# Optimization experiments

Measured on AMD Instinct MI355X. Metric: run time of the kernel, lower is better.

The kernel has to match this reference:

```python
import jax, jax.numpy as jnp
import numpy as np
import math

B, L, S, D = 4, 4096, 4096, 256
EPS = 1e-5

def _layernorm(x, g, b):
    mu = jnp.mean(x, axis=-1, keepdims=True)
    var = jnp.mean(jnp.square(x - mu), axis=-1, keepdims=True)
    return (x - mu) * jax.lax.rsqrt(var + EPS) * g + b

def setup_inputs() -> dict:
    key = jax.random.key(0)
    ks = jax.random.split(key, 14)
    s = 1.0 / math.sqrt(D)
    s2 = 1.0 / math.sqrt(2 * D)
    inp = {
        "source": jax.random.normal(ks[0], (B, L, D), jnp.float32),
        "target": jax.random.normal(ks[1], (B, S, D), jnp.float32),
        # linear weights stored as [in, out]
        "Wq": jax.random.uniform(ks[2], (D, D), jnp.float32, -s, s),
        "bq": jnp.zeros((D,), jnp.float32),
        "Wk": jax.random.uniform(ks[3], (D, D), jnp.float32, -s, s),
        "bk": jnp.zeros((D,), jnp.float32),
        "Wv": jax.random.uniform(ks[4], (D, D), jnp.float32, -s, s),
        "bv": jnp.zeros((D,), jnp.float32),
        "Wm": jax.random.uniform(ks[5], (D, D), jnp.float32, -s, s),
        "bm": jnp.zeros((D,), jnp.float32),
        "g1": jnp.ones((D,), jnp.float32),
        "beta1": jnp.zeros((D,), jnp.float32),
        "W1": jax.random.uniform(ks[6], (2 * D, 2 * D), jnp.float32, -s2, s2),
        "W2": jax.random.uniform(ks[7], (2 * D, D), jnp.float32, -s2, s2),
        "g2": jnp.ones((D,), jnp.float32),
        "beta2": jnp.zeros((D,), jnp.float32),
    }
    return inp

def reference(source, target, Wq, bq, Wk, bk, Wv, bv, Wm, bm, g1, beta1, W1, W2, g2, beta2):
    q = source @ Wq + bq              # [B, L, D]
    k = target @ Wk + bk              # [B, S, D]
    v = target @ Wv + bv              # [B, S, D]
    scale = 1.0 / math.sqrt(D)
    scores = jnp.einsum("bld,bsd->bls", q, k) * scale   # [B, L, S] materialized, as in source
    attn = jax.nn.softmax(scores, axis=-1)
    message = jnp.einsum("bls,bsd->bld", attn, v)        # [B, L, D]
    message = message @ Wm + bm
    message = _layernorm(message, g1, beta1)
    h = jnp.concatenate([source, message], axis=-1)      # [B, L, 2D]
    h = jax.nn.gelu(h @ W1, approximate=False)           # torch GELU is exact erf
    message = _layernorm(h @ W2, g2, beta2)
    return source + message
```

## Files before the change

### kernel.cpp

```cpp
#include <hip/hip_runtime.h>

typedef __bf16 bf16x8 __attribute__((ext_vector_type(8)));
typedef float f32x16 __attribute__((ext_vector_type(16)));
typedef float f32x4 __attribute__((ext_vector_type(4)));
typedef unsigned int u32;
typedef unsigned int u32x4 __attribute__((ext_vector_type(4)));
typedef unsigned short u16;
typedef unsigned short u16x4 __attribute__((ext_vector_type(4)));
typedef unsigned short u16x8 __attribute__((ext_vector_type(8)));

#define DEV static __device__ __forceinline__
#define AS1 __attribute__((address_space(1)))
#define AS3 __attribute__((address_space(3)))

DEV u16 f2bf(float f){
  unsigned u = __float_as_uint(f);
  u += 0x7FFFu + ((u >> 16) & 1u);
  return (u16)(u >> 16);
}
DEV float bf2f(u16 h){ return __uint_as_float(((u32)h) << 16); }

DEV void stage16(const u16* gsrc, const u16* ldst){
  __builtin_amdgcn_global_load_lds((const AS1 u32*)(unsigned long long)gsrc,
                                   (AS3 u32*)(u32)(unsigned long long)ldst,
                                   16, 0, 0);
}

constexpr int BATCH = 4, LQ = 4096, SK = 4096, DH = 256, BL = BATCH * LQ;
constexpr int NHALF = 2;
constexpr int ITERS = SK / NHALF / 64;

__global__ void prep_weights(const float* __restrict__ Wq, const float* __restrict__ Wk,
                             const float* __restrict__ Wv, const float* __restrict__ Wm,
                             const float* __restrict__ W1, const float* __restrict__ W2,
                             const float* __restrict__ bk, const float* __restrict__ bv,
                             u16* __restrict__ WqT, u16* __restrict__ WkvT,
                             u16* __restrict__ WmT,
                             u16* __restrict__ W1T, u16* __restrict__ W2T,
                             float* __restrict__ bkv){
  int idx = blockIdx.x * 256 + threadIdx.x;
  if (idx < 262144){
    int which = idx >> 16, i2 = idx & 65535;
    int r = i2 >> 8, c = i2 & 255;
    const float* S = (which==0)?Wq:(which==1)?Wk:(which==2)?Wv:Wm;
    u16*         D = (which==0)?WqT:(which==1)?WkvT:(which==2)?(WkvT+65536):WmT;
    D[c*256 + r] = f2bf(S[i2]);
  } else if (idx < 524288){
    int i2 = idx - 262144;
    int r = i2 >> 9, c = i2 & 511;
    W1T[c*512 + r] = f2bf(W1[i2]);
  } else if (idx < 655360){
    int i2 = idx - 524288;
    int r = i2 >> 8, c = i2 & 255;
    W2T[(size_t)c*512 + r] = f2bf(W2[i2]);
  } else if (idx < 655872){
    int i2 = idx - 655360;
    bkv[i2] = (i2 < 256) ? bk[i2] : bv[i2 - 256];
  }
}

template<bool A_F32, int EPI, bool WH>
__global__ __launch_bounds__(256, 2) void gemm128(
  const void* __restrict__ Ap, int lda, const u16* __restrict__ BTp,
  const float* __restrict__ bias, void* __restrict__ outp, void* __restrict__ outp2,
  u16* __restrict__ hcat,
  int M, int N, int K, float scale)
{
  __shared__ u16 A_lds[128 * 64];
  __shared__ u16 B_lds[128 * 64];
  const int tid = threadIdx.x, lane = tid & 63, wid = tid >> 6;
  const int ql = lane & 31, g = lane >> 5;
  const int m0 = blockIdx.y * 128, n0 = blockIdx.x * 128;
  const int mr = (wid & 1) * 64, nr = (wid >> 1) * 64;

  f32x16 acc[2][2] = {};
  f32x4 afreg[8];
  u32x4 abreg[4];
  u32x4 breg[4];
  const float* Af = (const float*)Ap;
  const u16*   Ab = (const u16*)Ap;

#define G_LOAD_A(kb) do { \
    if constexpr (A_F32){ \
      _Pragma("unroll") \
      for (int i = 0; i < 8; i++){ int item = tid + i*256; int r = item>>4, c = (item&15)*4; \
        afreg[i] = *(const f32x4*)&Af[(size_t)(m0+r)*lda + (kb)*64 + c]; } \
    } else { \
      _Pragma("unroll") \
      for (int i = 0; i < 4; i++){ int item = tid + i*256; int r = item>>3, c = (item&7)*8; \
        abreg[i] = *(const u32x4*)&Ab[(size_t)(m0+r)*lda + (kb)*64 + c]; } \
    } \
  } while(0)
#define G_LOAD_B(kb) do { \
    _Pragma("unroll") \
    for (int i = 0; i < 4; i++){ int item = tid + i*256; int r = item>>3, c = (item&7)*8; \
      breg[i] = *(const u32x4*)&BTp[(size_t)(n0+r)*K + (kb)*64 + c]; } \
  } while(0)

  G_LOAD_A(0); G_LOAD_B(0);

  const int nkb = K >> 6;
  for (int kb = 0; kb < nkb; ++kb){
    __syncthreads();
    if constexpr (A_F32){
      #pragma unroll
      for (int i = 0; i < 8; i++){ int item = tid + i*256; int r = item>>4, c = (item&15)*4;
        u16x4 h; h[0]=f2bf(afreg[i][0]); h[1]=f2bf(afreg[i][1]);
                 h[2]=f2bf(afreg[i][2]); h[3]=f2bf(afreg[i][3]);
        *(u16x4*)&A_lds[r*64 + (c ^ ((r&7)*8))] = h;
        if constexpr (WH){
          if (n0 == 0) *(u16x4*)&hcat[(size_t)(m0+r)*512 + kb*64 + c] = h;
        }
      }
    } else {
      #pragma unroll
      for (int i = 0; i < 4; i++){ int item = tid + i*256; int r = item>>3, c = (item&7)*8;
        *(u32x4*)&A_lds[r*64 + (c ^ ((r&7)*8))] = abreg[i]; }
    }
    #pragma unroll
    for (int i = 0; i < 4; i++){ int item = tid + i*256; int r = item>>3, c = (item&7)*8;
      *(u32x4*)&B_lds[r*64 + (c ^ ((r&7)*8))] = breg[i]; }
    __syncthreads();
    if (kb + 1 < nkb){ G_LOAD_A(kb+1); G_LOAD_B(kb+1); }

    #pragma unroll
    for (int kk = 0; kk < 4; kk++){
      bf16x8 af[2], bf[2];
      #pragma unroll
      for (int mi = 0; mi < 2; mi++)
        af[mi] = __builtin_bit_cast(bf16x8,
          *(const u32x4*)&A_lds[(mr+mi*32+ql)*64 + ((kk*16+g*8) ^ ((ql&7)*8))]);
      #pragma unroll
      for (int ni = 0; ni < 2; ni++)
        bf[ni] = __builtin_bit_cast(bf16x8,
          *(const u32x4*)&B_lds[(nr+ni*32+ql)*64 + ((kk*16+g*8) ^ ((ql&7)*8))]);
      #pragma unroll
      for (int mi = 0; mi < 2; mi++)
        #pragma unroll
        for (int ni = 0; ni < 2; ni++)
          acc[mi][ni] = __builtin_amdgcn_mfma_f32_32x32x16_bf16(af[mi], bf[ni], acc[mi][ni], 0, 0, 0);
    }
  }

  #pragma unroll
  for (int mi = 0; mi < 2; mi++){
    #pragma unroll
    for (int ni = 0; ni < 2; ni++){
      const int col = n0 + nr + ni*32 + ql;
      const float bv = bias ? bias[col] : 0.f;
      if constexpr (EPI == 4){
        if (col < 256){
          #pragma unroll
          for (int j = 0; j < 16; j++){
            int row = m0 + mr + mi*32 + (j&3) + 8*(j>>2) + 4*g;
            ((u16*)outp)[(size_t)row*256 + col] = f2bf(acc[mi][ni][j] + bv);
          }
        } else {
          const int col2 = col - 256;
          #pragma unroll
          for (int qd = 0; qd < 4; qd++){
            u16x4 h;
            #pragma unroll
            for (int i = 0; i < 4; i++) h[i] = f2bf(acc[mi][ni][qd*4+i] + bv);
            int row0 = m0 + mr + mi*32 + qd*8 + 4*g;
            int bb = row0 >> 12, ss = row0 & 4095;
            *(u16x4*)&((u16*)outp2)[((size_t)bb*DH + col2)*SK + ss] = h;
          }
        }
      } else {
        #pragma unroll
        for (int j = 0; j < 16; j++){
          int row = m0 + mr + mi*32 + (j&3) + 8*(j>>2) + 4*g;
          ((u16*)outp)[(size_t)row*N + col] = f2bf((acc[mi][ni][j] + bv) * scale);
        }
      }
    }
  }
}

__global__ __launch_bounds__(256, 2) void gemm_ln_wm(
  const u16* __restrict__ opart, const float* __restrict__ stats,
  const u16* __restrict__ BTp, const float* __restrict__ bias,
  const float* __restrict__ gamma, const float* __restrict__ beta,
  u16* __restrict__ outp)
{
  constexpr int K = 256;
  __shared__ __align__(16) char smem[36864];
  u16* A_lds = (u16*)smem;
  u16* B_lds = (u16*)(smem + 4096);
  float* scratch = (float*)smem;

  const int tid = threadIdx.x, lane = tid & 63, wid = tid >> 6;
  const int ql = lane & 31, g = lane >> 5;
  const int m0 = blockIdx.x * 32;
  const int ar = tid >> 3, ac = (tid & 7) * 8;

  float winv;
  { int row = m0 + ar;
    winv = 1.f / (stats[row] + stats[(size_t)BL + row]); }

  f32x16 acc[2] = {};
  u32x4 areg, areg2;
  u32x4 breg[8];

#define WM_LOAD_A(kb) do { \
    areg  = *(const u32x4*)&opart[(size_t)(m0+ar)*DH + (kb)*64 + ac]; \
    areg2 = *(const u32x4*)&opart[(size_t)BL*DH + (size_t)(m0+ar)*DH + (kb)*64 + ac]; \
  } while(0)
#define WM_LOAD_B(kb) do { \
    _Pragma("unroll") \
    for (int i = 0; i < 8; i++){ int item = tid + i*256; int r = item>>3, c = (item&7)*8; \
      breg[i] = *(const u32x4*)&BTp[(size_t)r*K + (kb)*64 + c]; } \
  } while(0)

  WM_LOAD_A(0); WM_LOAD_B(0);

  const int nkb = K >> 6;
  for (int kb = 0; kb < nkb; ++kb){
    __syncthreads();
    { u16x8 h;
      #pragma unroll
      for (int e = 0; e < 8; e++){
        u16 h0 = (u16)(areg[e>>1]  >> ((e&1)*16));
        u16 h1 = (u16)(areg2[e>>1] >> ((e&1)*16));
        h[e] = f2bf((bf2f(h0) + bf2f(h1)) * winv);
      }
      *(u16x8*)&A_lds[ar*64 + (ac ^ ((ar&7)*8))] = h; }
    #pragma unroll
    for (int i = 0; i < 8; i++){ int item = tid + i*256; int r = item>>3, c = (item&7)*8;
      *(u32x4*)&B_lds[r*64 + (c ^ ((r&7)*8))] = breg[i]; }
    __syncthreads();
    if (kb + 1 < nkb){ WM_LOAD_A(kb+1); WM_LOAD_B(kb+1); }

    #pragma unroll
    for (int kk = 0; kk < 4; kk++){
      bf16x8 af = __builtin_bit_cast(bf16x8,
        *(const u32x4*)&A_lds[ql*64 + ((kk*16+g*8) ^ ((ql&7)*8))]);
      #pragma unroll
      for (int ni = 0; ni < 2; ni++){
        bf16x8 bf = __builtin_bit_cast(bf16x8,
          *(const u32x4*)&B_lds[(wid*64+ni*32+ql)*64 + ((kk*16+g*8) ^ ((ql&7)*8))]);
        acc[ni] = __builtin_amdgcn_mfma_f32_32x32x16_bf16(af, bf, acc[ni], 0, 0, 0);
      }
    }
  }

  __syncthreads();

  float bv0 = bias[wid*64 + ql], bv1 = bias[wid*64 + 32 + ql];
  #pragma unroll
  for (int ni = 0; ni < 2; ni++)
    #pragma unroll
    for (int j = 0; j < 16; j++){
      int row = (j&3) + 8*(j>>2) + 4*g;
      scratch[row*257 + wid*64 + ni*32 + ql] = acc[ni][j] + (ni ? bv1 : bv0);
    }
  __syncthreads();

  f32x4 gv = *(const f32x4*)&gamma[lane*4];
  f32x4 bvv = *(const f32x4*)&beta[lane*4];
  #pragma unroll
  for (int rr = 0; rr < 8; rr++){
    const int row = wid*8 + rr;
    f32x4 v = *(const f32x4*)&scratch[row*257 + lane*4];
    float s1 = v[0]+v[1]+v[2]+v[3];
    float s2 = v[0]*v[0]+v[1]*v[1]+v[2]*v[2]+v[3]*v[3];
    #pragma unroll
    for (int m = 1; m < 64; m <<= 1){ s1 += __shfl_xor(s1, m, 64); s2 += __shfl_xor(s2, m, 64); }
    float mu = s1 * (1.f/DH);
    float var = s2 * (1.f/DH) - mu*mu;
    float rstd = rsqrtf(var + 1e-5f);
    u16x4 h;
    #pragma unroll
    for (int i = 0; i < 4; i++) h[i] = f2bf((v[i]-mu)*rstd*gv[i] + bvv[i]);
    *(u16x4*)&outp[(size_t)(m0+row)*512 + 256 + lane*4] = h;
  }
}

__global__ __launch_bounds__(256, 2) void fused_mlp(
  const u16* __restrict__ hcat, const u16* __restrict__ W1T,
  const u16* __restrict__ W2T, const float* __restrict__ gamma,
  const float* __restrict__ beta, const float* __restrict__ src,
  float* __restrict__ outp)
{
  __shared__ __align__(16) char smem[69632];
  u16* A1 = (u16*)smem;
  u16* B1 = (u16*)(smem + 4096);
  u16* Hl = (u16*)smem;
  u16* B2 = (u16*)(smem + 36864);
  float* scratch = (float*)smem;

  const int tid = threadIdx.x, lane = tid & 63, wid = tid >> 6;
  const int ql = lane & 31, g = lane >> 5;
  const int m0 = blockIdx.x * 32;

  f32x16 acc1[4] = {};
  for (int kb = 0; kb < 8; ++kb){
    if (kb) __syncthreads();
    { int r = tid >> 3, slot = tid & 7;
      stage16(&hcat[(size_t)(m0+r)*512 + kb*64 + ((slot ^ (r&7))<<3)],
              &A1[tid*8]); }
    #pragma unroll
    for (int i = 0; i < 16; i++){
      int grp = tid + i*256; int r = grp>>3, slot = grp&7;
      stage16(&W1T[(size_t)r*512 + kb*64 + ((slot ^ (r&7))<<3)], &B1[grp*8]);
    }
    __syncthreads();
    #pragma unroll
    for (int kk = 0; kk < 4; kk++){
      bf16x8 af = __builtin_bit_cast(bf16x8,
        *(const u32x4*)&A1[ql*64 + ((kk*16+g*8) ^ ((ql&7)*8))]);
      #pragma unroll
      for (int ni = 0; ni < 4; ni++){
        int rB = wid*128 + ni*32 + ql;
        bf16x8 bf = __builtin_bit_cast(bf16x8,
          *(const u32x4*)&B1[rB*64 + ((kk*16+g*8) ^ ((rB&7)*8))]);
        acc1[ni] = __builtin_amdgcn_mfma_f32_32x32x16_bf16(af, bf, acc1[ni], 0, 0, 0);
      }
    }
  }
  __syncthreads();

  #pragma unroll
  for (int ni = 0; ni < 4; ni++){
    const int col = wid*128 + ni*32 + ql;
    const int s = col >> 3;
    #pragma unroll
    for (int j = 0; j < 16; j++){
      int row = (j&3) + 8*(j>>2) + 4*g;
      float v = acc1[ni][j];
      v = 0.5f * v * (1.f + erff(v * 0.70710678118f));
      Hl[row*512 + ((s ^ (row&7))<<3) + (col&7)] = f2bf(v);
    }
  }
  __syncthreads();

  f32x16 acc2[2] = {};
  for (int kb = 0; kb < 8; ++kb){
    if (kb) __syncthreads();
    #pragma unroll
    for (int i = 0; i < 8; i++){
      int grp = tid + i*256; int r = grp>>3, slot = grp&7;
      stage16(&W2T[(size_t)r*512 + kb*64 + ((slot ^ (r&7))<<3)], &B2[grp*8]);
    }
    __syncthreads();
    #pragma unroll
    for (int kk = 0; kk < 4; kk++){
      int c0 = kb*64 + kk*16 + g*8;
      bf16x8 af = __builtin_bit_cast(bf16x8,
        *(const u32x4*)&Hl[ql*512 + (((c0>>3) ^ (ql&7))<<3)]);
      #pragma unroll
      for (int ni = 0; ni < 2; ni++){
        int rB = wid*64 + ni*32 + ql;
        bf16x8 bf = __builtin_bit_cast(bf16x8,
          *(const u32x4*)&B2[rB*64 + ((kk*16+g*8) ^ ((rB&7)*8))]);
        acc2[ni] = __builtin_amdgcn_mfma_f32_32x32x16_bf16(af, bf, acc2[ni], 0, 0, 0);
      }
    }
  }
  __syncthreads();

  #pragma unroll
  for (int ni = 0; ni < 2; ni++)
    #pragma unroll
    for (int j = 0; j < 16; j++){
      int row = (j&3) + 8*(j>>2) + 4*g;
      scratch[row*257 + wid*64 + ni*32 + ql] = acc2[ni][j];
    }
  __syncthreads();

  f32x4 gv = *(const f32x4*)&gamma[lane*4];
  f32x4 bvv = *(const f32x4*)&beta[lane*4];
  #pragma unroll
  for (int rr = 0; rr < 8; rr++){
    const int row = wid*8 + rr;
    f32x4 v = *(const f32x4*)&scratch[row*257 + lane*4];
    float s1 = v[0]+v[1]+v[2]+v[3];
    float s2 = v[0]*v[0]+v[1]*v[1]+v[2]*v[2]+v[3]*v[3];
    #pragma unroll
    for (int m = 1; m < 64; m <<= 1){ s1 += __shfl_xor(s1, m, 64); s2 += __shfl_xor(s2, m, 64); }
    float mu = s1 * (1.f/DH);
    float var = s2 * (1.f/DH) - mu*mu;
    float rstd = rsqrtf(var + 1e-5f);
    f32x4 s = *(const f32x4*)&src[(size_t)(m0+row)*DH + lane*4];
    f32x4 o;
    #pragma unroll
    for (int i = 0; i < 4; i++) o[i] = s[i] + (v[i]-mu)*rstd*gv[i] + bvv[i];
    *(f32x4*)&outp[(size_t)(m0+row)*DH + lane*4] = o;
  }
}

__global__ __launch_bounds__(512, 2) void attn_kernel(
  const u16* __restrict__ qb, const u16* __restrict__ kb,
  const u16* __restrict__ vtb, u16* __restrict__ opart, float* __restrict__ stats)
{
  __shared__ u16 K_lds[2][64 * 256];
  __shared__ u16 VT_lds[2][256 * 64];
  __shared__ u32x4 P_exch[4][4][64];
  __shared__ float L_exch[4][2][32];

  const int tid = threadIdx.x;
  const int wid = tid >> 6, lane = tid & 63;
  const int ql = lane & 31, g = lane >> 5;
  const int qpair = wid >> 1, sh = wid & 1;
  const int b = blockIdx.y, half = blockIdx.z;
  const int qrow0 = blockIdx.x * 128 + qpair * 32;
  const int s0base = half * (SK / NHALF);

  const u16* kbase = kb  + (size_t)b * SK * DH;
  const u16* vbase = vtb + (size_t)b * DH * SK;

#define STAGE_K(bi, s0) do { \
    _Pragma("unroll") \
    for (int i = 0; i < 4; i++){ \
      int grp = tid + i*512; int s = grp>>5, slot = grp&31; \
      stage16(kbase + (size_t)((s0)+s)*DH + ((slot ^ (s&31))<<3), \
              &K_lds[bi][(i*512 + wid*64)*8]); \
    } } while(0)
#define STAGE_V(bi, s0) do { \
    _Pragma("unroll") \
    for (int i = 0; i < 4; i++){ \
      int grp = tid + i*512; int d = grp>>3, slot = grp&7; \
      stage16(vbase + (size_t)d*SK + (s0) + ((slot ^ (d&7))<<3), \
              &VT_lds[bi][(i*512 + wid*64)*8]); \
    } } while(0)

  STAGE_K(0, s0base);
  STAGE_V(0, s0base);

  bf16x8 qf[16];
  {
    const u16* qp = qb + ((size_t)(b*LQ + qrow0 + ql)) * DH + g * 8;
    #pragma unroll
    for (int kk = 0; kk < 16; kk++)
      qf[kk] = __builtin_bit_cast(bf16x8, *(const u32x4*)(qp + kk*16));
  }

  f32x16 accO[4] = {};
  float l_lane = 0.f;

  __syncthreads();

  for (int it = 0; it < ITERS; ++it){
    const int cur = it & 1;
    if (it + 1 < ITERS){
      STAGE_K(cur ^ 1, s0base + (it+1)*64);
      STAGE_V(cur ^ 1, s0base + (it+1)*64);
    }

    f32x16 ps = {};
    __builtin_amdgcn_s_setprio(1);
    #pragma unroll
    for (int kk = 0; kk < 16; ++kk){
      bf16x8 kf = __builtin_bit_cast(bf16x8,
        *(const u32x4*)&K_lds[cur][(sh*32+ql)*256 + (((kk*2+g) ^ ql)<<3)]);
      ps = __builtin_amdgcn_mfma_f32_32x32x16_bf16(kf, qf[kk], ps, 0, 0, 0);
    }
    __builtin_amdgcn_s_setprio(0);

    #pragma unroll
    for (int j = 0; j < 16; j++) ps[j] = exp2f(ps[j]);
    float s8[8];
    #pragma unroll
    for (int j = 0; j < 8; j++) s8[j] = ps[j] + ps[j+8];
    l_lane += ((s8[0]+s8[4]) + (s8[1]+s8[5])) + ((s8[2]+s8[6]) + (s8[3]+s8[7]));

    u32 Wp[4][2];
    #pragma unroll
    for (int qd = 0; qd < 4; qd++)
      #pragma unroll
      for (int h = 0; h < 2; h++){
        float lo = ps[qd*4 + 2*h], hi = ps[qd*4 + 2*h + 1];
        asm("v_cvt_pk_bf16_f32 %0, %1, %2" : "=v"(Wp[qd][h]) : "v"(lo), "v"(hi));
      }
    #pragma unroll
    for (int i = 0; i < 2; i++){
      const int qp2 = i * 2;
      u32 a0 = Wp[qp2][0], b0 = Wp[qp2+1][0];
      u32 a1 = Wp[qp2][1], b1 = Wp[qp2+1][1];
      asm("v_permlane32_swap_b32 %0, %1" : "+v"(a0), "+v"(b0));
      asm("v_permlane32_swap_b32 %0, %1" : "+v"(a1), "+v"(b1));
      u32x4 w; w[0] = a0; w[1] = a1; w[2] = b0; w[3] = b1;
      P_exch[qpair][sh*2 + i][lane] = w;
    }

    asm volatile("s_waitcnt lgkmcnt(0)" ::: "memory");
    __builtin_amdgcn_s_barrier();
    __builtin_amdgcn_sched_barrier(0);

    bf16x8 pf0 = __builtin_bit_cast(bf16x8, P_exch[qpair][0][lane]);
    bf16x8 pf1 = __builtin_bit_cast(bf16x8, P_exch[qpair][1][lane]);
    bf16x8 pf2 = __builtin_bit_cast(bf16x8, P_exch[qpair][2][lane]);
    bf16x8 pf3 = __builtin_bit_cast(bf16x8, P_exch[qpair][3][lane]);

    __builtin_amdgcn_s_setprio(1);
    #pragma unroll
    for (int dt = 0; dt < 4; dt++){
      const int dtg = sh*4 + dt;
      bf16x8 vf0 = __builtin_bit_cast(bf16x8,
        *(const u32x4*)&VT_lds[cur][(dtg*32+ql)*64 + (((0*2+g) ^ (ql&7))<<3)]);
      accO[dt] = __builtin_amdgcn_mfma_f32_32x32x16_bf16(vf0, pf0, accO[dt], 0, 0, 0);
      bf16x8 vf1 = __builtin_bit_cast(bf16x8,
        *(const u32x4*)&VT_lds[cur][(dtg*32+ql)*64 + (((1*2+g) ^ (ql&7))<<3)]);
      accO[dt] = __builtin_amdgcn_mfma_f32_32x32x16_bf16(vf1, pf1, accO[dt], 0, 0, 0);
      bf16x8 vf2 = __builtin_bit_cast(bf16x8,
        *(const u32x4*)&VT_lds[cur][(dtg*32+ql)*64 + (((2*2+g) ^ (ql&7))<<3)]);
      accO[dt] = __builtin_amdgcn_mfma_f32_32x32x16_bf16(vf2, pf2, accO[dt], 0, 0, 0);
      bf16x8 vf3 = __builtin_bit_cast(bf16x8,
        *(const u32x4*)&VT_lds[cur][(dtg*32+ql)*64 + (((3*2+g) ^ (ql&7))<<3)]);
      accO[dt] = __builtin_amdgcn_mfma_f32_32x32x16_bf16(vf3, pf3, accO[dt], 0, 0, 0);
    }
    __builtin_amdgcn_s_setprio(0);

    asm volatile("s_waitcnt vmcnt(0) lgkmcnt(0)" ::: "memory");
    __builtin_amdgcn_s_barrier();
    __builtin_amdgcn_sched_barrier(0);
  }

  float l_run = l_lane + __shfl_xor(l_lane, 32, 64);
  if (g == 0) L_exch[qpair][sh][ql] = l_run;
  __syncthreads();
  float l_tot = l_run + L_exch[qpair][sh^1][ql];

  const int rowb = b * LQ + qrow0;
  if (sh == 0 && g == 0)
    stats[(size_t)half*BL + rowb + ql] = l_tot;

  float* scratch = (float*)&K_lds[0][0] + wid * 1056;
  #pragma unroll
  for (int dt = 0; dt < 4; dt++){
    const int dtg = sh*4 + dt;
    #pragma unroll
    for (int j = 0; j < 16; j++){
      int dl = (j&3) + 8*(j>>2) + 4*g;
      scratch[ql*33 + dl] = accO[dt][j];
    }
    int q2 = lane >> 1, dl2 = (lane & 1) * 16;
    u16x8 h0, h1;
    #pragma unroll
    for (int i = 0; i < 8; i++){ h0[i] = f2bf(scratch[q2*33 + dl2 + i]);
                                 h1[i] = f2bf(scratch[q2*33 + dl2 + 8 + i]); }
    u16* op = &opart[((size_t)half*BL + rowb + q2)*DH + dtg*32 + dl2];
    *(u16x8*)op = h0;
    *(u16x8*)(op + 8) = h1;
  }
}

extern "C" void kernel_launch(void* const* d_in, const int* in_sizes, int n_in,
                              void* d_out, int out_size, void* d_ws, size_t ws_size,
                              hipStream_t stream)
{
  const float* source = (const float*)d_in[0];
  const float* target = (const float*)d_in[1];
  const float* Wq = (const float*)d_in[2];  const float* bq = (const float*)d_in[3];
  const float* Wk = (const float*)d_in[4];  const float* bk = (const float*)d_in[5];
  const float* Wv = (const float*)d_in[6];  const float* bv = (const float*)d_in[7];
  const float* Wm = (const float*)d_in[8];  const float* bm = (const float*)d_in[9];
  const float* g1 = (const float*)d_in[10]; const float* be1 = (const float*)d_in[11];
  const float* W1 = (const float*)d_in[12]; const float* W2 = (const float*)d_in[13];
  const float* g2 = (const float*)d_in[14]; const float* be2 = (const float*)d_in[15];

  char* ws = (char*)d_ws;
  u16* WqT  = (u16*)(ws);
  u16* WkvT = (u16*)(ws + (size_t)(1u<<17));
  u16* WmT  = (u16*)(ws + (size_t)3*(1u<<17));
  u16* W1T  = (u16*)(ws + (size_t)4*(1u<<17));
  u16* W2T  = (u16*)(ws + (size_t)8*(1u<<17));
  float* bkv = (float*)(ws + (size_t)10*(1u<<17));
  size_t off = (size_t)10*(1u<<17) + 4096;
  u16* qbuf  = (u16*)(ws + off); off += (size_t)BL*DH*2;
  u16* kbuf  = (u16*)(ws + off); off += (size_t)BL*DH*2;
  u16* vtbuf = (u16*)(ws + off); off += (size_t)BL*DH*2;
  u16* hcat  = (u16*)(ws + off); off += (size_t)BL*512*2;
  u16* opart = (u16*)(ws + off); off += (size_t)NHALF*BL*DH*2;
  float* stats = (float*)(ws + off); off += (size_t)NHALF*BL*4;

  prep_weights<<<dim3(2562), 256, 0, stream>>>(Wq, Wk, Wv, Wm, W1, W2, bk, bv,
                                               WqT, WkvT, WmT, W1T, W2T, bkv);

  const float qscale = 1.4426950408889634f / 16.0f;
  gemm128<true, 0, true><<<dim3(2, BL/128), 256, 0, stream>>>(
      source, 256, WqT, bq, qbuf, nullptr, hcat, BL, 256, 256, qscale);
  gemm128<true, 4, false><<<dim3(4, BL/128), 256, 0, stream>>>(
      target, 256, WkvT, bkv, kbuf, vtbuf, nullptr, BL, 512, 256, 1.0f);

  attn_kernel<<<dim3(LQ/128, BATCH, NHALF), 512, 0, stream>>>(qbuf, kbuf, vtbuf, opart, stats);

  gemm_ln_wm<<<dim3(BL/32), 256, 0, stream>>>(opart, stats, WmT, bm, g1, be1, hcat);

  fused_mlp<<<dim3(BL/32), 256, 0, stream>>>(hcat, W1T, W2T, g2, be2, source,
                                             (float*)d_out);
}
```

Before: 162.8 us.

## Merge Q and KV projection launches; double row tile in Wm and MLP kernels

The separate Q and KV projection GEMM launches become one qkv_gemm launch. Blocks pick source/Wq or target/Wkv from blockIdx.x, which cuts one launch and fills the GPU better. The Wm+LayerNorm and fused MLP kernels move from 32-row, 256-thread blocks to 64-row, 512-thread blocks, so each weight tile staged into LDS is reused across twice as many rows. The cost is larger LDS use (up to 96KB) and bigger blocks, which may lower occupancy and halves the grid size.

```diff
diff --git a/kernel.cpp b/kernel.cpp
--- a/kernel.cpp
+++ b/kernel.cpp
@@ -59,69 +59,57 @@
   }
 }
 
-template<bool A_F32, int EPI, bool WH>
-__global__ __launch_bounds__(256, 2) void gemm128(
-  const void* __restrict__ Ap, int lda, const u16* __restrict__ BTp,
-  const float* __restrict__ bias, void* __restrict__ outp, void* __restrict__ outp2,
-  u16* __restrict__ hcat,
-  int M, int N, int K, float scale)
+__global__ __launch_bounds__(256, 2) void qkv_gemm(
+  const float* __restrict__ src, const float* __restrict__ tgt,
+  const u16* __restrict__ WqT, const u16* __restrict__ WkvT,
+  const float* __restrict__ bq, const float* __restrict__ bkv,
+  u16* __restrict__ qbuf, u16* __restrict__ kbuf, u16* __restrict__ vtbuf,
+  u16* __restrict__ hcat, float qscale)
 {
   __shared__ u16 A_lds[128 * 64];
   __shared__ u16 B_lds[128 * 64];
   const int tid = threadIdx.x, lane = tid & 63, wid = tid >> 6;
   const int ql = lane & 31, g = lane >> 5;
-  const int m0 = blockIdx.y * 128, n0 = blockIdx.x * 128;
+  const bool isQ = blockIdx.x < 2;
+  const int m0 = blockIdx.y * 128;
+  const int n0 = (isQ ? blockIdx.x : (blockIdx.x - 2)) * 128;
   const int mr = (wid & 1) * 64, nr = (wid >> 1) * 64;
+  const float* Af = isQ ? src : tgt;
+  const u16* BTp = isQ ? WqT : WkvT;
+  const float* bias = isQ ? bq : bkv;
+  const bool wh = isQ && (blockIdx.x == 0);
 
   f32x16 acc[2][2] = {};
   f32x4 afreg[8];
-  u32x4 abreg[4];
   u32x4 breg[4];
-  const float* Af = (const float*)Ap;
-  const u16*   Ab = (const u16*)Ap;
-
-#define G_LOAD_A(kb) do { \
-    if constexpr (A_F32){ \
-      _Pragma("unroll") \
-      for (int i = 0; i < 8; i++){ int item = tid + i*256; int r = item>>4, c = (item&15)*4; \
-        afreg[i] = *(const f32x4*)&Af[(size_t)(m0+r)*lda + (kb)*64 + c]; } \
-    } else { \
-      _Pragma("unroll") \
-      for (int i = 0; i < 4; i++){ int item = tid + i*256; int r = item>>3, c = (item&7)*8; \
-        abreg[i] = *(const u32x4*)&Ab[(size_t)(m0+r)*lda + (kb)*64 + c]; } \
-    } \
+
+#define QK_LOAD_A(kb) do { \
+    _Pragma("unroll") \
+    for (int i = 0; i < 8; i++){ int item = tid + i*256; int r = item>>4, c = (item&15)*4; \
+      afreg[i] = *(const f32x4*)&Af[(size_t)(m0+r)*256 + (kb)*64 + c]; } \
   } while(0)
-#define G_LOAD_B(kb) do { \
+#define QK_LOAD_B(kb) do { \
     _Pragma("unroll") \
     for (int i = 0; i < 4; i++){ int item = tid + i*256; int r = item>>3, c = (item&7)*8; \
-      breg[i] = *(const u32x4*)&BTp[(size_t)(n0+r)*K + (kb)*64 + c]; } \
+      breg[i] = *(const u32x4*)&BTp[(size_t)(n0+r)*256 + (kb)*64 + c]; } \
   } while(0)
 
-  G_LOAD_A(0); G_LOAD_B(0);
-
-  const int nkb = K >> 6;
-  for (int kb = 0; kb < nkb; ++kb){
+  QK_LOAD_A(0); QK_LOAD_B(0);
+
+  for (int kb = 0; kb < 4; ++kb){
     __syncthreads();
-    if constexpr (A_F32){
-      #pragma unroll
-      for (int i = 0; i < 8; i++){ int item = tid + i*256; int r = item>>4, c = (item&15)*4;
-        u16x4 h; h[0]=f2bf(afreg[i][0]); h[1]=f2bf(afreg[i][1]);
-                 h[2]=f2bf(afreg[i][2]); h[3]=f2bf(afreg[i][3]);
-        *(u16x4*)&A_lds[r*64 + (c ^ ((r&7)*8))] = h;
-        if constexpr (WH){
-          if (n0 == 0) *(u16x4*)&hcat[(size_t)(m0+r)*512 + kb*64 + c] = h;
-        }
-      }
-    } else {
-      #pragma unroll
-      for (int i = 0; i < 4; i++){ int item = tid + i*256; int r = item>>3, c = (item&7)*8;
-        *(u32x4*)&A_lds[r*64 + (c ^ ((r&7)*8))] = abreg[i]; }
+    #pragma unroll
+    for (int i = 0; i < 8; i++){ int item = tid + i*256; int r = item>>4, c = (item&15)*4;
+      u16x4 h; h[0]=f2bf(afreg[i][0]); h[1]=f2bf(afreg[i][1]);
+               h[2]=f2bf(afreg[i][2]); h[3]=f2bf(afreg[i][3]);
+      *(u16x4*)&A_lds[r*64 + (c ^ ((r&7)*8))] = h;
+      if (wh) *(u16x4*)&hcat[(size_t)(m0+r)*512 + kb*64 + c] = h;
     }
     #pragma unroll
     for (int i = 0; i < 4; i++){ int item = tid + i*256; int r = item>>3, c = (item&7)*8;
       *(u32x4*)&B_lds[r*64 + (c ^ ((r&7)*8))] = breg[i]; }
     __syncthreads();
-    if (kb + 1 < nkb){ G_LOAD_A(kb+1); G_LOAD_B(kb+1); }
+    if (kb + 1 < 4){ QK_LOAD_A(kb+1); QK_LOAD_B(kb+1); }
 
     #pragma unroll
     for (int kk = 0; kk < 4; kk++){
@@ -147,52 +135,49 @@
     #pragma unroll
     for (int ni = 0; ni < 2; ni++){
       const int col = n0 + nr + ni*32 + ql;
-      const float bv = bias ? bias[col] : 0.f;
-      if constexpr (EPI == 4){
-        if (col < 256){
-          #pragma unroll
-          for (int j = 0; j < 16; j++){
-            int row = m0 + mr + mi*32 + (j&3) + 8*(j>>2) + 4*g;
-            ((u16*)outp)[(size_t)row*256 + col] = f2bf(acc[mi][ni][j] + bv);
-          }
-        } else {
-          const int col2 = col - 256;
-          #pragma unroll
-          for (int qd = 0; qd < 4; qd++){
-            u16x4 h;
-            #pragma unroll
-            for (int i = 0; i < 4; i++) h[i] = f2bf(acc[mi][ni][qd*4+i] + bv);
-            int row0 = m0 + mr + mi*32 + qd*8 + 4*g;
-            int bb = row0 >> 12, ss = row0 & 4095;
-            *(u16x4*)&((u16*)outp2)[((size_t)bb*DH + col2)*SK + ss] = h;
-          }
-        }
-      } else {
+      const float bv = bias[col];
+      if (isQ){
         #pragma unroll
         for (int j = 0; j < 16; j++){
           int row = m0 + mr + mi*32 + (j&3) + 8*(j>>2) + 4*g;
-          ((u16*)outp)[(size_t)row*N + col] = f2bf((acc[mi][ni][j] + bv) * scale);
+          qbuf[(size_t)row*256 + col] = f2bf((acc[mi][ni][j] + bv) * qscale);
+        }
+      } else if (col < 256){
+        #pragma unroll
+        for (int j = 0; j < 16; j++){
+          int row = m0 + mr + mi*32 + (j&3) + 8*(j>>2) + 4*g;
+          kbuf[(size_t)row*256 + col] = f2bf(acc[mi][ni][j] + bv);
+        }
+      } else {
+        const int col2 = col - 256;
+        #pragma unroll
+        for (int qd = 0; qd < 4; qd++){
+          u16x4 h;
+          #pragma unroll
+          for (int i = 0; i < 4; i++) h[i] = f2bf(acc[mi][ni][qd*4+i] + bv);
+          int row0 = m0 + mr + mi*32 + qd*8 + 4*g;
+          int bb = row0 >> 12, ss = row0 & 4095;
+          *(u16x4*)&vtbuf[((size_t)bb*DH + col2)*SK + ss] = h;
         }
       }
     }
   }
 }
 
-__global__ __launch_bounds__(256, 2) void gemm_ln_wm(
+__global__ __launch_bounds__(512, 2) void gemm_ln_wm(
   const u16* __restrict__ opart, const float* __restrict__ stats,
   const u16* __restrict__ BTp, const float* __restrict__ bias,
   const float* __restrict__ gamma, const float* __restrict__ beta,
   u16* __restrict__ outp)
 {
-  constexpr int K = 256;
-  __shared__ __align__(16) char smem[36864];
+  __shared__ __align__(16) char smem[65792];
   u16* A_lds = (u16*)smem;
-  u16* B_lds = (u16*)(smem + 4096);
+  u16* B_lds = (u16*)(smem + 8192);
   float* scratch = (float*)smem;
 
   const int tid = threadIdx.x, lane = tid & 63, wid = tid >> 6;
   const int ql = lane & 31, g = lane >> 5;
-  const int m0 = blockIdx.x * 32;
+  const int m0 = blockIdx.x * 64;
   const int ar = tid >> 3, ac = (tid & 7) * 8;
 
   float winv;
@@ -201,7 +186,7 @@
 
   f32x16 acc[2] = {};
   u32x4 areg, areg2;
-  u32x4 breg[8];
+  u32x4 breg[4];
 
 #define WM_LOAD_A(kb) do { \
     areg  = *(const u32x4*)&opart[(size_t)(m0+ar)*DH + (kb)*64 + ac]; \
@@ -209,14 +194,13 @@
   } while(0)
 #define WM_LOAD_B(kb) do { \
     _Pragma("unroll") \
-    for (int i = 0; i < 8; i++){ int item = tid + i*256; int r = item>>3, c = (item&7)*8; \
-      breg[i] = *(const u32x4*)&BTp[(size_t)r*K + (kb)*64 + c]; } \
+    for (int i = 0; i < 4; i++){ int item = tid + i*512; int r = item>>3, c = (item&7)*8; \
+      breg[i] = *(const u32x4*)&BTp[(size_t)r*256 + (kb)*64 + c]; } \
   } while(0)
 
   WM_LOAD_A(0); WM_LOAD_B(0);
 
-  const int nkb = K >> 6;
-  for (int kb = 0; kb < nkb; ++kb){
+  for (int kb = 0; kb < 4; ++kb){
     __syncthreads();
     { u16x8 h;
       #pragma unroll
@@ -227,33 +211,35 @@
       }
       *(u16x8*)&A_lds[ar*64 + (ac ^ ((ar&7)*8))] = h; }
     #pragma unroll
-    for (int i = 0; i < 8; i++){ int item = tid + i*256; int r = item>>3, c = (item&7)*8;
+    for (int i = 0; i < 4; i++){ int item = tid + i*512; int r = item>>3, c = (item&7)*8;
       *(u32x4*)&B_lds[r*64 + (c ^ ((r&7)*8))] = breg[i]; }
     __syncthreads();
-    if (kb + 1 < nkb){ WM_LOAD_A(kb+1); WM_LOAD_B(kb+1); }
+    if (kb + 1 < 4){ WM_LOAD_A(kb+1); WM_LOAD_B(kb+1); }
 
     #pragma unroll
     for (int kk = 0; kk < 4; kk++){
-      bf16x8 af = __builtin_bit_cast(bf16x8,
-        *(const u32x4*)&A_lds[ql*64 + ((kk*16+g*8) ^ ((ql&7)*8))]);
-      #pragma unroll
-      for (int ni = 0; ni < 2; ni++){
-        bf16x8 bf = __builtin_bit_cast(bf16x8,
-          *(const u32x4*)&B_lds[(wid*64+ni*32+ql)*64 + ((kk*16+g*8) ^ ((ql&7)*8))]);
-        acc[ni] = __builtin_amdgcn_mfma_f32_32x32x16_bf16(af, bf, acc[ni], 0, 0, 0);
-      }
-    }
-  }
-
-  __syncthreads();
-
-  float bv0 = bias[wid*64 + ql], bv1 = bias[wid*64 + 32 + ql];
-  #pragma unroll
-  for (int ni = 0; ni < 2; ni++)
+      bf16x8 af[2];
+      #pragma unroll
+      for (int mi = 0; mi < 2; mi++)
+        af[mi] = __builtin_bit_cast(bf16x8,
+          *(const u32x4*)&A_lds[(mi*32+ql)*64 + ((kk*16+g*8) ^ ((ql&7)*8))]);
+      bf16x8 bf = __builtin_bit_cast(bf16x8,
+        *(const u32x4*)&B_lds[(wid*32+ql)*64 + ((kk*16+g*8) ^ ((ql&7)*8))]);
+      #pragma unroll
+      for (int mi = 0; mi < 2; mi++)
+        acc[mi] = __builtin_amdgcn_mfma_f32_32x32x16_bf16(af[mi], bf, acc[mi], 0, 0, 0);
+    }
+  }
+
+  __syncthreads();
+
+  const float bv = bias[wid*32 + ql];
+  #pragma unroll
+  for (int mi = 0; mi < 2; mi++)
     #pragma unroll
     for (int j = 0; j < 16; j++){
-      int row = (j&3) + 8*(j>>2) + 4*g;
-      scratch[row*257 + wid*64 + ni*32 + ql] = acc[ni][j] + (ni ? bv1 : bv0);
+      int row = mi*32 + (j&3) + 8*(j>>2) + 4*g;
+      scratch[row*257 + wid*32 + ql] = acc[mi][j] + bv;
     }
   __syncthreads();
 
@@ -277,95 +263,105 @@
   }
 }
 
-__global__ __launch_bounds__(256, 2) void fused_mlp(
+__global__ __launch_bounds__(512, 2) void fused_mlp(
   const u16* __restrict__ hcat, const u16* __restrict__ W1T,
   const u16* __restrict__ W2T, const float* __restrict__ gamma,
   const float* __restrict__ beta, const float* __restrict__ src,
   float* __restrict__ outp)
 {
-  __shared__ __align__(16) char smem[69632];
+  __shared__ __align__(16) char smem[98304];
   u16* A1 = (u16*)smem;
-  u16* B1 = (u16*)(smem + 4096);
+  u16* B1 = (u16*)(smem + 8192);
   u16* Hl = (u16*)smem;
-  u16* B2 = (u16*)(smem + 36864);
+  u16* B2 = (u16*)(smem + 65536);
   float* scratch = (float*)smem;
 
   const int tid = threadIdx.x, lane = tid & 63, wid = tid >> 6;
   const int ql = lane & 31, g = lane >> 5;
-  const int m0 = blockIdx.x * 32;
-
-  f32x16 acc1[4] = {};
+  const int m0 = blockIdx.x * 64;
+
+  f32x16 acc1[2][2] = {};
   for (int kb = 0; kb < 8; ++kb){
     if (kb) __syncthreads();
     { int r = tid >> 3, slot = tid & 7;
       stage16(&hcat[(size_t)(m0+r)*512 + kb*64 + ((slot ^ (r&7))<<3)],
               &A1[tid*8]); }
     #pragma unroll
-    for (int i = 0; i < 16; i++){
-      int grp = tid + i*256; int r = grp>>3, slot = grp&7;
+    for (int i = 0; i < 8; i++){
+      int grp = tid + i*512; int r = grp>>3, slot = grp&7;
       stage16(&W1T[(size_t)r*512 + kb*64 + ((slot ^ (r&7))<<3)], &B1[grp*8]);
     }
     __syncthreads();
     #pragma unroll
     for (int kk = 0; kk < 4; kk++){
-      bf16x8 af = __builtin_bit_cast(bf16x8,
-        *(const u32x4*)&A1[ql*64 + ((kk*16+g*8) ^ ((ql&7)*8))]);
-      #pragma unroll
-      for (int ni = 0; ni < 4; ni++){
-        int rB = wid*128 + ni*32 + ql;
+      bf16x8 af[2];
+      #pragma unroll
+      for (int mi = 0; mi < 2; mi++)
+        af[mi] = __builtin_bit_cast(bf16x8,
+          *(const u32x4*)&A1[(mi*32+ql)*64 + ((kk*16+g*8) ^ ((ql&7)*8))]);
+      #pragma unroll
+      for (int ni = 0; ni < 2; ni++){
+        int rB = wid*64 + ni*32 + ql;
         bf16x8 bf = __builtin_bit_cast(bf16x8,
-          *(const u32x4*)&B1[rB*64 + ((kk*16+g*8) ^ ((rB&7)*8))]);
-        acc1[ni] = __builtin_amdgcn_mfma_f32_32x32x16_bf16(af, bf, acc1[ni], 0, 0, 0);
+          *(const u32x4*)&B1[rB*64 + ((kk*16+g*8) ^ ((ql&7)*8))]);
+        #pragma unroll
+        for (int mi = 0; mi < 2; mi++)
+          acc1[mi][ni] = __builtin_amdgcn_mfma_f32_32x32x16_bf16(af[mi], bf, acc1[mi][ni], 0, 0, 0);
       }
     }
   }
   __syncthreads();
 
   #pragma unroll
-  for (int ni = 0; ni < 4; ni++){
-    const int col = wid*128 + ni*32 + ql;
-    const int s = col >> 3;
-    #pragma unroll
-    for (int j = 0; j < 16; j++){
-      int row = (j&3) + 8*(j>>2) + 4*g;
-      float v = acc1[ni][j];
-      v = 0.5f * v * (1.f + erff(v * 0.70710678118f));
-      Hl[row*512 + ((s ^ (row&7))<<3) + (col&7)] = f2bf(v);
-    }
-  }
+  for (int mi = 0; mi < 2; mi++)
+    #pragma unroll
+    for (int ni = 0; ni < 2; ni++){
+      const int col = wid*64 + ni*32 + ql;
+      const int s = col >> 3;
+      #pragma unroll
+      for (int j = 0; j < 16; j++){
+        int row = mi*32 + (j&3) + 8*(j>>2) + 4*g;
+        float v = acc1[mi][ni][j];
+        v = 0.5f * v * (1.f + erff(v * 0.70710678118f));
+        Hl[row*512 + ((s ^ (row&7))<<3) + (col&7)] = f2bf(v);
+      }
+    }
   __syncthreads();
 
   f32x16 acc2[2] = {};
   for (int kb = 0; kb < 8; ++kb){
     if (kb) __syncthreads();
     #pragma unroll
-    for (int i = 0; i < 8; i++){
-      int grp = tid + i*256; int r = grp>>3, slot = grp&7;
+    for (int i = 0; i < 4; i++){
+      int grp = tid + i*512; int r = grp>>3, slot = grp&7;
       stage16(&W2T[(size_t)r*512 + kb*64 + ((slot ^ (r&7))<<3)], &B2[grp*8]);
     }
     __syncthreads();
     #pragma unroll
     for (int kk = 0; kk < 4; kk++){
-      int c0 = kb*64 + kk*16 + g*8;
-      bf16x8 af = __builtin_bit_cast(bf16x8,
-        *(const u32x4*)&Hl[ql*512 + (((c0>>3) ^ (ql&7))<<3)]);
-      #pragma unroll
-      for (int ni = 0; ni < 2; ni++){
-        int rB = wid*64 + ni*32 + ql;
-        bf16x8 bf = __builtin_bit_cast(bf16x8,
-          *(const u32x4*)&B2[rB*64 + ((kk*16+g*8) ^ ((rB&7)*8))]);
-        acc2[ni] = __builtin_amdgcn_mfma_f32_32x32x16_bf16(af, bf, acc2[ni], 0, 0, 0);
+      int c0s = (kb*64 + kk*16 + g*8) >> 3;
+      bf16x8 af[2];
+      #pragma unroll
+      for (int mi = 0; mi < 2; mi++){
+        int row = mi*32 + ql;
+        af[mi] = __builtin_bit_cast(bf16x8,
+          *(const u32x4*)&Hl[row*512 + ((c0s ^ (row&7))<<3)]);
       }
-    }
-  }
-  __syncthreads();
-
-  #pragma unroll
-  for (int ni = 0; ni < 2; ni++)
+      bf16x8 bf = __builtin_bit_cast(bf16x8,
+        *(const u32x4*)&B2[(wid*32+ql)*64 + ((kk*16+g*8) ^ ((ql&7)*8))]);
+      #pragma unroll
+      for (int mi = 0; mi < 2; mi++)
+        acc2[mi] = __builtin_amdgcn_mfma_f32_32x32x16_bf16(af[mi], bf, acc2[mi], 0, 0, 0);
+    }
+  }
+  __syncthreads();
+
+  #pragma unroll
+  for (int mi = 0; mi < 2; mi++)
     #pragma unroll
     for (int j = 0; j < 16; j++){
-      int row = (j&3) + 8*(j>>2) + 4*g;
-      scratch[row*257 + wid*64 + ni*32 + ql] = acc2[ni][j];
+      int row = mi*32 + (j&3) + 8*(j>>2) + 4*g;
+      scratch[row*257 + wid*32 + ql] = acc2[mi][j];
     }
   __syncthreads();
 
@@ -579,15 +575,13 @@
                                                WqT, WkvT, WmT, W1T, W2T, bkv);
 
   const float qscale = 1.4426950408889634f / 16.0f;
-  gemm128<true, 0, true><<<dim3(2, BL/128), 256, 0, stream>>>(
-      source, 256, WqT, bq, qbuf, nullptr, hcat, BL, 256, 256, qscale);
-  gemm128<true, 4, false><<<dim3(4, BL/128), 256, 0, stream>>>(
-      target, 256, WkvT, bkv, kbuf, vtbuf, nullptr, BL, 512, 256, 1.0f);
+  qkv_gemm<<<dim3(6, BL/128), 256, 0, stream>>>(
+      source, target, WqT, WkvT, bq, bkv, qbuf, kbuf, vtbuf, hcat, qscale);
 
   attn_kernel<<<dim3(LQ/128, BATCH, NHALF), 512, 0, stream>>>(qbuf, kbuf, vtbuf, opart, stats);
 
-  gemm_ln_wm<<<dim3(BL/32), 256, 0, stream>>>(opart, stats, WmT, bm, g1, be1, hcat);
-
-  fused_mlp<<<dim3(BL/32), 256, 0, stream>>>(hcat, W1T, W2T, g2, be2, source,
+  gemm_ln_wm<<<dim3(BL/64), 512, 0, stream>>>(opart, stats, WmT, bm, g1, be1, hcat);
+
+  fused_mlp<<<dim3(BL/64), 512, 0, stream>>>(hcat, W1T, W2T, g2, be2, source,
                                              (float*)d_out);
 }
```

After: 160.6 us (median of 2 runs). About the same (-1.3%).
